# Performance work log

Measured on AMD Instinct MI355X. Metric: run time of the kernel, lower is better.

The kernel has to match this reference:

```python
import jax, jax.numpy as jnp
import numpy as np

B, N, D_MODEL, HIDDEN, ACTION_BIN = 4096, 8, 1024, 2048, 256


def setup_inputs() -> dict:
    key = jax.random.key(0)
    k_x, k_w1, k_b1, k_w2, k_b2 = jax.random.split(key, 5)
    # per-action-dim MLP weights stacked along leading n axis
    s1 = 1.0 / np.sqrt(D_MODEL)
    s2 = 1.0 / np.sqrt(HIDDEN)
    return {
        "x": jax.random.normal(k_x, (B, N, D_MODEL), dtype=jnp.float32),
        "W1": jax.random.normal(k_w1, (N, D_MODEL, HIDDEN), dtype=jnp.float32) * s1,
        "b1": jax.random.normal(k_b1, (N, HIDDEN), dtype=jnp.float32) * s1,
        "W2": jax.random.normal(k_w2, (N, HIDDEN, ACTION_BIN), dtype=jnp.float32) * s2,
        "b2": jax.random.normal(k_b2, (N, ACTION_BIN), dtype=jnp.float32) * s2,
    }


def reference(x, W1, b1, W2, b2):
    # Original torch module loops over n slices, each with its own
    # Linear(d_model->hidden) -> ReLU -> Linear(hidden->action_bin).
    # Equivalent grouped/batched matmul over the n axis:
    x = x.astype(jnp.float32)
    h = jnp.einsum('bnd,ndh->bnh', x, W1) + b1[None, :, :]   # [b, n, hidden]
    h = jax.nn.relu(h)
    out = jnp.einsum('bnh,nha->bna', h, W2) + b2[None, :, :]  # [b, n, action_bin]
    return out
```

## Files before the change

kernel.cpp:

```cpp
#include <hip/hip_runtime.h>
#include <stdint.h>

#define BTOT   4096
#define NGRP   8
#define DMODEL 1024
#define HIDDEN 2048
#define ABIN   256

typedef short bf16x8 __attribute__((ext_vector_type(8)));
typedef float f32x4  __attribute__((ext_vector_type(4)));

__device__ __forceinline__ ushort f2bf(float f) {
    union { float f; uint32_t u; } v; v.f = f;
    return (ushort)((v.u + 0x7FFFu + ((v.u >> 16) & 1u)) >> 16);
}

__device__ __forceinline__ void gl_lds16(const ushort* g, ushort* l) {
    __builtin_amdgcn_global_load_lds(
        (const __attribute__((address_space(1))) uint32_t*)g,
        (__attribute__((address_space(3))) uint32_t*)l,
        16, 0, 0);
}

#define W1_TILES ((DMODEL / 32) * (HIDDEN / 32))
#define W2_TILES ((HIDDEN / 32) * (ABIN / 32))
__global__ void transpose_w12(const float* __restrict__ W1, ushort* __restrict__ W1t,
                              const float* __restrict__ W2, ushort* __restrict__ W2t)
{
    __shared__ float tl[32][33];
    const int n = blockIdx.y;
    const float* W; ushort* Wt; int K, N, bx;
    if (blockIdx.x < W1_TILES) {
        W = W1; Wt = W1t; K = DMODEL; N = HIDDEN; bx = blockIdx.x;
    } else {
        W = W2; Wt = W2t; K = HIDDEN; N = ABIN;  bx = blockIdx.x - W1_TILES;
    }
    const int nt = bx % (N / 32);
    const int kt = bx / (N / 32);
    const float* Wn  = W  + (size_t)n * K * N;
    ushort*      Wtn = Wt + (size_t)n * N * K;
    const int tx = threadIdx.x & 31, ty = threadIdx.x >> 5;
#pragma unroll
    for (int j = 0; j < 4; j++)
        tl[ty + 8 * j][tx] = Wn[(size_t)(kt * 32 + ty + 8 * j) * N + nt * 32 + tx];
    __syncthreads();
#pragma unroll
    for (int j = 0; j < 4; j++) {
        const int r = ty + 8 * j;
        Wtn[(size_t)(nt * 32 + r) * K + kt * 32 + tx] = f2bf(tl[tx][r]);
    }
}

__global__ void conv_x(const float* __restrict__ x, ushort* __restrict__ xb,
                       int CH, int cb)
{
    const int flat = blockIdx.x * 256 + threadIdx.x;
    const int d8 = flat & 127;
    const int rem = flat >> 7;
    const int n = rem & 7;
    const int r = rem >> 3;
    const float* src = x + ((size_t)(cb + r) * NGRP + n) * DMODEL + d8 * 8;
    float4 v0 = *(const float4*)(src);
    float4 v1 = *(const float4*)(src + 4);
    bf16x8 p;
    p[0] = (short)f2bf(v0.x); p[1] = (short)f2bf(v0.y);
    p[2] = (short)f2bf(v0.z); p[3] = (short)f2bf(v0.w);
    p[4] = (short)f2bf(v1.x); p[5] = (short)f2bf(v1.y);
    p[6] = (short)f2bf(v1.z); p[7] = (short)f2bf(v1.w);
    *(bf16x8*)(xb + ((size_t)n * CH + r) * DMODEL + d8 * 8) = p;
}

#define REGN(buf,op,half,ks) (sm + ((((buf)*2+(op))*2+(half))*2+(ks))*4096)

template<int MH>
__device__ __forceinline__ void mma_q(f32x4 (&acc)[8][4], const bf16x8 (&af)[4],
                                      const bf16x8 (&bv)[4])
{
#pragma unroll
    for (int m4 = 0; m4 < 4; ++m4)
#pragma unroll
        for (int nf = 0; nf < 4; ++nf)
            acc[MH * 4 + m4][nf] = __builtin_amdgcn_mfma_f32_16x16x32_bf16(
                af[m4], bv[nf], acc[MH * 4 + m4][nf], 0, 0, 0);
}

__global__ __launch_bounds__(512, 2)
void gemm8_1(const ushort* __restrict__ A, const ushort* __restrict__ Bt,
             const float* __restrict__ bias, ushort* __restrict__ h, int CH)
{
    constexpr int K = DMODEL, NDIM = HIDDEN, KT = K / 64;
    const int MT = CH >> 8, NT = NDIM >> 8;
    extern __shared__ ushort sm[];

    const int nwg = gridDim.x;
    const int bid = blockIdx.x;
    const int swz = (bid & 7) * (nwg >> 3) + (bid >> 3);
    const int n   = swz / (MT * NT);
    const int rem = swz - n * (MT * NT);
    const int mt  = rem / NT;
    const int nt  = rem - mt * NT;

    const int tid = threadIdx.x;
    const int l = tid & 63, wid = tid >> 6;
    const int wr = wid >> 2, wc = wid & 3, wc2 = wc >> 1;
    const int lq = l >> 4, lr = l & 15;

    const ushort* Ab = A  + ((size_t)n * CH   + (size_t)mt * 256) * K;
    const ushort* Bb = Bt + ((size_t)n * NDIM + (size_t)nt * 256) * K;

    const int srow = tid >> 2;
    const int sseg = (tid & 3) ^ ((tid >> 3) & 3);

    auto stageA = [&](int b, int T, int ks) {
        const size_t kofs = (size_t)T * 64 + ks * 32 + sseg * 8;
        gl_lds16(Ab + (size_t)srow * K + kofs,         REGN(b, 0, 0, ks) + tid * 8);
        gl_lds16(Ab + (size_t)(128 + srow) * K + kofs, REGN(b, 0, 1, ks) + tid * 8);
    };
    auto stageB = [&](int b, int T, int ks) {
        const size_t kofs = (size_t)T * 64 + ks * 32 + sseg * 8;
        gl_lds16(Bb + (size_t)srow * K + kofs,         REGN(b, 1, 0, ks) + tid * 8);
        gl_lds16(Bb + (size_t)(128 + srow) * K + kofs, REGN(b, 1, 1, ks) + tid * 8);
    };
    auto ldA = [&](bf16x8 (&af)[4], int b, int kk, int mh) {
#pragma unroll
        for (int m4 = 0; m4 < 4; ++m4) {
            const int rh = mh * 64 + m4 * 16 + lr;
            af[m4] = *(const bf16x8*)(REGN(b, 0, wr, kk) + rh * 32 + (lq ^ ((rh >> 1) & 3)) * 8);
        }
    };
    auto ldB = [&](bf16x8 (&bv)[4], int b, int kk) {
#pragma unroll
        for (int nf = 0; nf < 4; ++nf) {
            const int rb = (wc & 1) * 64 + nf * 16 + lr;
            bv[nf] = *(const bf16x8*)(REGN(b, 1, wc2, kk) + rb * 32 + (lq ^ ((rb >> 1) & 3)) * 8);
        }
    };

    f32x4 acc[8][4];
#pragma unroll
    for (int i = 0; i < 8; ++i)
#pragma unroll
        for (int j = 0; j < 4; ++j) acc[i][j] = (f32x4){0.f, 0.f, 0.f, 0.f};

    stageA(0, 0, 0); stageB(0, 0, 0); stageA(0, 0, 1); stageB(0, 0, 1);
    asm volatile("s_waitcnt vmcnt(4)" ::: "memory");
    __builtin_amdgcn_s_barrier();

    bf16x8 aX[4], aY[4], bv0[4], bv1[4];
    ldA(aX, 0, 0, 0); ldB(bv0, 0, 0);

    for (int g = 0; g < KT; ++g) {
        const int c = g & 1;
        const bool ns = (g + 1 < KT);

        ldA(aY, c, 0, 1);
        if (ns) stageA(c ^ 1, g + 1, 0);
        asm volatile("s_waitcnt lgkmcnt(4)" ::: "memory");
        __builtin_amdgcn_sched_barrier(0);
        __builtin_amdgcn_s_setprio(1);
        mma_q<0>(acc, aX, bv0);
        __builtin_amdgcn_s_setprio(0);
        if (ns) asm volatile("s_waitcnt vmcnt(2)" ::: "memory");
        else    asm volatile("s_waitcnt vmcnt(0)" ::: "memory");
        __builtin_amdgcn_s_barrier();

        ldA(aX, c, 1, 0); ldB(bv1, c, 1);
        if (ns) stageB(c ^ 1, g + 1, 0);
        asm volatile("s_waitcnt lgkmcnt(8)" ::: "memory");
        __builtin_amdgcn_sched_barrier(0);
        __builtin_amdgcn_s_setprio(1);
        mma_q<1>(acc, aY, bv0);
        __builtin_amdgcn_s_setprio(0);
        __builtin_amdgcn_s_barrier();

        ldA(aY, c, 1, 1);
        if (ns) stageA(c ^ 1, g + 1, 1);
        asm volatile("s_waitcnt lgkmcnt(4)" ::: "memory");
        __builtin_amdgcn_sched_barrier(0);
        __builtin_amdgcn_s_setprio(1);
        mma_q<0>(acc, aX, bv1);
        __builtin_amdgcn_s_setprio(0);
        __builtin_amdgcn_s_barrier();

        if (ns) stageB(c ^ 1, g + 1, 1);
        asm volatile("s_waitcnt lgkmcnt(0)" ::: "memory");
        __builtin_amdgcn_sched_barrier(0);
        __builtin_amdgcn_s_setprio(1);
        mma_q<1>(acc, aY, bv1);
        __builtin_amdgcn_s_setprio(0);
        if (ns) asm volatile("s_waitcnt vmcnt(4)" ::: "memory");
        __builtin_amdgcn_s_barrier();
        if (ns) { ldA(aX, c ^ 1, 0, 0); ldB(bv0, c ^ 1, 0); }
    }

    __builtin_amdgcn_sched_barrier(0);

    float bias4[4];
#pragma unroll
    for (int nf = 0; nf < 4; ++nf)
        bias4[nf] = bias[(size_t)n * NDIM + nt * 256 + wc * 64 + nf * 16 + lr];
#pragma unroll
    for (int m = 0; m < 8; ++m) {
#pragma unroll
        for (int r = 0; r < 4; ++r) {
            const int row = mt * 256 + wr * 128 + m * 16 + lq * 4 + r;
            ushort* dst = h + ((size_t)n * CH + row) * HIDDEN + nt * 256 + wc * 64 + lr;
#pragma unroll
            for (int nf = 0; nf < 4; ++nf)
                dst[nf * 16] = f2bf(fmaxf(acc[m][nf][r] + bias4[nf], 0.f));
        }
    }
}

__global__ __launch_bounds__(256, 4)
void gemm2(const ushort* __restrict__ A, const ushort* __restrict__ Bt,
           const float* __restrict__ bias, float* __restrict__ outp,
           int CH, int cb)
{
    constexpr int K = HIDDEN, NDIM = ABIN, NT = NDIM / 128, BK = 64;
    __shared__ __align__(16) ushort As[128 * BK];
    __shared__ __align__(16) ushort Bs[128 * BK];

    const int n  = blockIdx.y;
    const int mt = blockIdx.x / NT;
    const int nt = blockIdx.x % NT;

    const ushort* Ab = A  + ((size_t)n * CH   + mt * 128) * K;
    const ushort* Bb = Bt + ((size_t)n * NDIM + nt * 128) * K;

    const int t = threadIdx.x, l = t & 63, w = t >> 6;
    const int wr = w >> 1, wc = w & 1;
    const int lq = l >> 4, lr = l & 15;

    f32x4 acc[4][4];
#pragma unroll
    for (int i = 0; i < 4; i++)
#pragma unroll
        for (int j = 0; j < 4; j++) acc[i][j] = (f32x4){0.f, 0.f, 0.f, 0.f};

    for (int ki = 0; ki < K / BK; ++ki) {
        const ushort* Ak = Ab + ki * BK;
        const ushort* Bk = Bb + ki * BK;
        __syncthreads();
#pragma unroll
        for (int i = 0; i < 4; i++) {
            const int flat = t + 256 * i;
            const int row = flat >> 3;
            const int seg = (flat & 7) ^ (row & 7);
            gl_lds16(Ak + (size_t)row * K + seg * 8, (ushort*)As + flat * 8);
            gl_lds16(Bk + (size_t)row * K + seg * 8, (ushort*)Bs + flat * 8);
        }
        __syncthreads();

#pragma unroll
        for (int kk = 0; kk < 2; kk++) {
            bf16x8 af[4], bf[4];
#pragma unroll
            for (int m = 0; m < 4; m++) {
                const int row = wr * 64 + m * 16 + lr;
                af[m] = *(const bf16x8*)&As[row * BK + ((kk * 4 + lq) ^ (row & 7)) * 8];
            }
#pragma unroll
            for (int nf = 0; nf < 4; nf++) {
                const int row = wc * 64 + nf * 16 + lr;
                bf[nf] = *(const bf16x8*)&Bs[row * BK + ((kk * 4 + lq) ^ (row & 7)) * 8];
            }
#pragma unroll
            for (int m = 0; m < 4; m++)
#pragma unroll
                for (int nf = 0; nf < 4; nf++)
                    acc[m][nf] = __builtin_amdgcn_mfma_f32_16x16x32_bf16(af[m], bf[nf], acc[m][nf], 0, 0, 0);
        }
    }

#pragma unroll
    for (int nf = 0; nf < 4; nf++) {
        const int colg = nt * 128 + wc * 64 + nf * 16 + lr;
        const float bv = bias[(size_t)n * NDIM + colg];
#pragma unroll
        for (int m = 0; m < 4; m++) {
#pragma unroll
            for (int r = 0; r < 4; r++) {
                const int row = mt * 128 + wr * 64 + m * 16 + lq * 4 + r;
                outp[((size_t)(cb + row) * NGRP + n) * ABIN + colg] = acc[m][nf][r] + bv;
            }
        }
    }
}

extern "C" void kernel_launch(void* const* d_in, const int* in_sizes, int n_in,
                              void* d_out, int out_size, void* d_ws, size_t ws_size,
                              hipStream_t stream)
{
    const float* x  = (const float*)d_in[0];
    const float* W1 = (const float*)d_in[1];
    const float* b1 = (const float*)d_in[2];
    const float* W2 = (const float*)d_in[3];
    const float* b2 = (const float*)d_in[4];

    hipFuncSetAttribute((const void*)gemm8_1,
                        hipFuncAttributeMaxDynamicSharedMemorySize, 131072);

    ushort* W1t = (ushort*)d_ws;
    ushort* W2t = W1t + (size_t)NGRP * HIDDEN * DMODEL;
    ushort* xb  = W2t + (size_t)NGRP * ABIN * HIDDEN;
    const size_t fixed = ((size_t)NGRP * HIDDEN * DMODEL + (size_t)NGRP * ABIN * HIDDEN) * 2;

    int CH = 4096;
    while (CH > 256 && fixed + (size_t)CH * (NGRP * (DMODEL + HIDDEN) * 2) > ws_size) CH >>= 1;
    ushort* h = xb + (size_t)NGRP * CH * DMODEL;

    {
        dim3 g(W1_TILES + W2_TILES, NGRP);
        transpose_w12<<<g, 256, 0, stream>>>(W1, W1t, W2, W2t);
    }

    for (int cb = 0; cb < BTOT; cb += CH) {
        conv_x<<<CH * 4, 256, 0, stream>>>(x, xb, CH, cb);
        const int g1 = NGRP * (CH / 256) * (HIDDEN / 256);
        gemm8_1<<<g1, 512, 131072, stream>>>(xb, W1t, b1, h, CH);
        dim3 g2((CH / 128) * (ABIN / 128), NGRP);
        gemm2<<<g2, 256, 0, stream>>>(h, W2t, b2, (float*)d_out, CH, cb);
    }
}
```

Baseline: 255.5 us.

## Fuse fp32-to-bf16 conversion of x into first GEMM's A-tile staging

Removes the separate conv_x kernel. The first GEMM now loads fp32 x directly into registers, converts it with v_cvt_pk_bf16_f32, and writes the bf16 values into LDS, with the pipeline waitcnts reworked around this. This drops one kernel launch and the bf16 x round-trip through workspace. In exchange it reads twice the A bytes per tile (fp32), re-reads x once per HIDDEN tile (8 times), uses more registers, and loses the async global_load_lds path for A.

```diff
diff --git a/kernel.cpp b/kernel.cpp
--- a/kernel.cpp
+++ b/kernel.cpp
@@ -51,25 +51,6 @@
     }
 }
 
-__global__ void conv_x(const float* __restrict__ x, ushort* __restrict__ xb,
-                       int CH, int cb)
-{
-    const int flat = blockIdx.x * 256 + threadIdx.x;
-    const int d8 = flat & 127;
-    const int rem = flat >> 7;
-    const int n = rem & 7;
-    const int r = rem >> 3;
-    const float* src = x + ((size_t)(cb + r) * NGRP + n) * DMODEL + d8 * 8;
-    float4 v0 = *(const float4*)(src);
-    float4 v1 = *(const float4*)(src + 4);
-    bf16x8 p;
-    p[0] = (short)f2bf(v0.x); p[1] = (short)f2bf(v0.y);
-    p[2] = (short)f2bf(v0.z); p[3] = (short)f2bf(v0.w);
-    p[4] = (short)f2bf(v1.x); p[5] = (short)f2bf(v1.y);
-    p[6] = (short)f2bf(v1.z); p[7] = (short)f2bf(v1.w);
-    *(bf16x8*)(xb + ((size_t)n * CH + r) * DMODEL + d8 * 8) = p;
-}
-
 #define REGN(buf,op,half,ks) (sm + ((((buf)*2+(op))*2+(half))*2+(ks))*4096)
 
 template<int MH>
@@ -85,8 +66,9 @@
 }
 
 __global__ __launch_bounds__(512, 2)
-void gemm8_1(const ushort* __restrict__ A, const ushort* __restrict__ Bt,
-             const float* __restrict__ bias, ushort* __restrict__ h, int CH)
+void gemm8_1(const float* __restrict__ X, const ushort* __restrict__ Bt,
+             const float* __restrict__ bias, ushort* __restrict__ h,
+             int CH, int cb)
 {
     constexpr int K = DMODEL, NDIM = HIDDEN, KT = K / 64;
     const int MT = CH >> 8, NT = NDIM >> 8;
@@ -105,16 +87,31 @@
     const int wr = wid >> 2, wc = wid & 3, wc2 = wc >> 1;
     const int lq = l >> 4, lr = l & 15;
 
-    const ushort* Ab = A  + ((size_t)n * CH   + (size_t)mt * 256) * K;
     const ushort* Bb = Bt + ((size_t)n * NDIM + (size_t)nt * 256) * K;
 
     const int srow = tid >> 2;
     const int sseg = (tid & 3) ^ ((tid >> 3) & 3);
 
-    auto stageA = [&](int b, int T, int ks) {
+    const float* Xr0 = X + ((size_t)(cb + mt * 256 +       srow) * NGRP + n) * DMODEL;
+    const float* Xr1 = X + ((size_t)(cb + mt * 256 + 128 + srow) * NGRP + n) * DMODEL;
+
+    auto aload4 = [&](float4 (&d)[4], int T, int ks) {
         const size_t kofs = (size_t)T * 64 + ks * 32 + sseg * 8;
-        gl_lds16(Ab + (size_t)srow * K + kofs,         REGN(b, 0, 0, ks) + tid * 8);
-        gl_lds16(Ab + (size_t)(128 + srow) * K + kofs, REGN(b, 0, 1, ks) + tid * 8);
+        d[0] = *(const float4*)(Xr0 + kofs); d[1] = *(const float4*)(Xr0 + kofs + 4);
+        d[2] = *(const float4*)(Xr1 + kofs); d[3] = *(const float4*)(Xr1 + kofs + 4);
+    };
+    auto awrite2 = [&](int b, int ks, const float4 (&d)[4]) {
+        uint32_t w0, w1, w2, w3;
+        asm("v_cvt_pk_bf16_f32 %0, %1, %2" : "=v"(w0) : "v"(d[0].x), "v"(d[0].y));
+        asm("v_cvt_pk_bf16_f32 %0, %1, %2" : "=v"(w1) : "v"(d[0].z), "v"(d[0].w));
+        asm("v_cvt_pk_bf16_f32 %0, %1, %2" : "=v"(w2) : "v"(d[1].x), "v"(d[1].y));
+        asm("v_cvt_pk_bf16_f32 %0, %1, %2" : "=v"(w3) : "v"(d[1].z), "v"(d[1].w));
+        *(uint4*)(REGN(b, 0, 0, ks) + tid * 8) = (uint4){w0, w1, w2, w3};
+        asm("v_cvt_pk_bf16_f32 %0, %1, %2" : "=v"(w0) : "v"(d[2].x), "v"(d[2].y));
+        asm("v_cvt_pk_bf16_f32 %0, %1, %2" : "=v"(w1) : "v"(d[2].z), "v"(d[2].w));
+        asm("v_cvt_pk_bf16_f32 %0, %1, %2" : "=v"(w2) : "v"(d[3].x), "v"(d[3].y));
+        asm("v_cvt_pk_bf16_f32 %0, %1, %2" : "=v"(w3) : "v"(d[3].z), "v"(d[3].w));
+        *(uint4*)(REGN(b, 0, 1, ks) + tid * 8) = (uint4){w0, w1, w2, w3};
     };
     auto stageB = [&](int b, int T, int ks) {
         const size_t kofs = (size_t)T * 64 + ks * 32 + sseg * 8;
@@ -142,39 +139,50 @@
 #pragma unroll
         for (int j = 0; j < 4; ++j) acc[i][j] = (f32x4){0.f, 0.f, 0.f, 0.f};
 
-    stageA(0, 0, 0); stageB(0, 0, 0); stageA(0, 0, 1); stageB(0, 0, 1);
-    asm volatile("s_waitcnt vmcnt(4)" ::: "memory");
+    float4 qa[4], ra[4];
+
+    aload4(qa, 0, 0); aload4(ra, 0, 1);
+    stageB(0, 0, 0); stageB(0, 0, 1);
+    asm volatile("s_waitcnt vmcnt(0)" ::: "memory");
+    awrite2(0, 0, qa); awrite2(0, 1, ra);
+    asm volatile("s_waitcnt lgkmcnt(0)" ::: "memory");
     __builtin_amdgcn_s_barrier();
 
     bf16x8 aX[4], aY[4], bv0[4], bv1[4];
     ldA(aX, 0, 0, 0); ldB(bv0, 0, 0);
+    __builtin_amdgcn_sched_barrier(0);
 
     for (int g = 0; g < KT; ++g) {
         const int c = g & 1;
         const bool ns = (g + 1 < KT);
 
+        if (ns) { aload4(qa, g + 1, 0); stageB(c ^ 1, g + 1, 0); }
         ldA(aY, c, 0, 1);
-        if (ns) stageA(c ^ 1, g + 1, 0);
         asm volatile("s_waitcnt lgkmcnt(4)" ::: "memory");
         __builtin_amdgcn_sched_barrier(0);
         __builtin_amdgcn_s_setprio(1);
         mma_q<0>(acc, aX, bv0);
         __builtin_amdgcn_s_setprio(0);
-        if (ns) asm volatile("s_waitcnt vmcnt(2)" ::: "memory");
+        if (ns) asm volatile("s_waitcnt vmcnt(6)" ::: "memory");
         else    asm volatile("s_waitcnt vmcnt(0)" ::: "memory");
         __builtin_amdgcn_s_barrier();
 
+        if (ns) {
+            aload4(ra, g + 1, 1);
+            asm volatile("s_waitcnt vmcnt(6)" ::: "memory");
+            awrite2(c ^ 1, 0, qa);
+        }
         ldA(aX, c, 1, 0); ldB(bv1, c, 1);
-        if (ns) stageB(c ^ 1, g + 1, 0);
-        asm volatile("s_waitcnt lgkmcnt(8)" ::: "memory");
+        if (ns) asm volatile("s_waitcnt lgkmcnt(10)" ::: "memory");
+        else    asm volatile("s_waitcnt lgkmcnt(8)" ::: "memory");
         __builtin_amdgcn_sched_barrier(0);
         __builtin_amdgcn_s_setprio(1);
         mma_q<1>(acc, aY, bv0);
         __builtin_amdgcn_s_setprio(0);
         __builtin_amdgcn_s_barrier();
 
+        if (ns) stageB(c ^ 1, g + 1, 1);
         ldA(aY, c, 1, 1);
-        if (ns) stageA(c ^ 1, g + 1, 1);
         asm volatile("s_waitcnt lgkmcnt(4)" ::: "memory");
         __builtin_amdgcn_sched_barrier(0);
         __builtin_amdgcn_s_setprio(1);
@@ -182,18 +190,19 @@
         __builtin_amdgcn_s_setprio(0);
         __builtin_amdgcn_s_barrier();
 
-        if (ns) stageB(c ^ 1, g + 1, 1);
+        if (ns) {
+            asm volatile("s_waitcnt vmcnt(2)" ::: "memory");
+            awrite2(c ^ 1, 1, ra);
+        }
         asm volatile("s_waitcnt lgkmcnt(0)" ::: "memory");
         __builtin_amdgcn_sched_barrier(0);
         __builtin_amdgcn_s_setprio(1);
         mma_q<1>(acc, aY, bv1);
         __builtin_amdgcn_s_setprio(0);
-        if (ns) asm volatile("s_waitcnt vmcnt(4)" ::: "memory");
         __builtin_amdgcn_s_barrier();
         if (ns) { ldA(aX, c ^ 1, 0, 0); ldB(bv0, c ^ 1, 0); }
-    }
-
-    __builtin_amdgcn_sched_barrier(0);
+        __builtin_amdgcn_sched_barrier(0);
+    }
 
     float bias4[4];
 #pragma unroll
@@ -303,12 +312,11 @@
 
     ushort* W1t = (ushort*)d_ws;
     ushort* W2t = W1t + (size_t)NGRP * HIDDEN * DMODEL;
-    ushort* xb  = W2t + (size_t)NGRP * ABIN * HIDDEN;
+    ushort* h   = W2t + (size_t)NGRP * ABIN * HIDDEN;
     const size_t fixed = ((size_t)NGRP * HIDDEN * DMODEL + (size_t)NGRP * ABIN * HIDDEN) * 2;
 
     int CH = 4096;
-    while (CH > 256 && fixed + (size_t)CH * (NGRP * (DMODEL + HIDDEN) * 2) > ws_size) CH >>= 1;
-    ushort* h = xb + (size_t)NGRP * CH * DMODEL;
+    while (CH > 256 && fixed + (size_t)CH * (NGRP * HIDDEN * 2) > ws_size) CH >>= 1;
 
     {
         dim3 g(W1_TILES + W2_TILES, NGRP);
@@ -316,9 +324,8 @@
     }
 
     for (int cb = 0; cb < BTOT; cb += CH) {
-        conv_x<<<CH * 4, 256, 0, stream>>>(x, xb, CH, cb);
         const int g1 = NGRP * (CH / 256) * (HIDDEN / 256);
-        gemm8_1<<<g1, 512, 131072, stream>>>(xb, W1t, b1, h, CH);
+        gemm8_1<<<g1, 512, 131072, stream>>>(x, W1t, b1, h, CH, cb);
         dim3 g2((CH / 128) * (ABIN / 128), NGRP);
         gemm2<<<g2, 256, 0, stream>>>(h, W2t, b2, (float*)d_out, CH, cb);
     }
```

New measurement: 300.7 us. 1.18x slower.
